# Optimization experiments

Measured on AMD Instinct MI355X. Metric: run time of the kernel, lower is better.

The kernel has to match this reference:

```python
import jax, jax.numpy as jnp
import numpy as np

N_NODES = 100000
N_EDGES = 1600000
IN_DIM = 64
HEADS = [4, 4]
DIMS = [16, 16]


def gat_layer(x, src, dst, W, al, ar, b, n_nodes):
    """DGL-style GATConv: x [N,F] -> [N,H,D]."""
    H, D = al.shape
    z = (x @ W).reshape(-1, H, D)                      # [N,H,D]
    el = jnp.sum(z * al, axis=-1)                      # [N,H]
    er = jnp.sum(z * ar, axis=-1)                      # [N,H]
    e = jax.nn.leaky_relu(el[src] + er[dst], 0.2)      # [E,H] edge scores
    # numerically-stable edge softmax over incoming edges of each dst node
    m = jax.ops.segment_max(e, dst, num_segments=n_nodes)
    m = jnp.where(jnp.isfinite(m), m, 0.0)
    ex = jnp.exp(e - jax.lax.stop_gradient(m)[dst])    # [E,H]
    denom = jax.ops.segment_sum(ex, dst, num_segments=n_nodes)
    alpha = ex / jnp.maximum(denom[dst], 1e-9)         # [E,H]
    # scatter-aggregate messages alpha * z[src]
    out = jax.ops.segment_sum(alpha[:, :, None] * z[src], dst, num_segments=n_nodes)
    return out + b.reshape(H, D)


def setup_inputs() -> dict:
    key = jax.random.key(0)
    ks = jax.random.split(key, 16)
    feat = jax.random.normal(ks[0], (N_NODES, IN_DIM), dtype=jnp.float32)
    src = jax.random.randint(ks[1], (N_EDGES,), 0, N_NODES, dtype=jnp.int32)
    dst = jax.random.randint(ks[2], (N_EDGES,), 0, N_NODES, dtype=jnp.int32)
    def lin(k, fi, fo):
        return jax.random.normal(k, (fi, fo), dtype=jnp.float32) * (1.0 / np.sqrt(fi))
    H0, D0 = HEADS[0], DIMS[0]
    H1, D1 = HEADS[1], DIMS[1]
    inp = {
        "feat": feat, "src": src, "dst": dst,
        "W0": lin(ks[3], IN_DIM, H0 * D0),
        "al0": jax.random.normal(ks[4], (H0, D0), jnp.float32) * 0.1,
        "ar0": jax.random.normal(ks[5], (H0, D0), jnp.float32) * 0.1,
        "b0": jnp.zeros((H0 * D0,), jnp.float32),
        "W1": lin(ks[6], H0 * D0, H1 * D1),
        "al1": jax.random.normal(ks[7], (H1, D1), jnp.float32) * 0.1,
        "ar1": jax.random.normal(ks[8], (H1, D1), jnp.float32) * 0.1,
        "b1": jnp.zeros((H1 * D1,), jnp.float32),
        "Wo": lin(ks[9], H1 * D1, 1),
        "alo": jax.random.normal(ks[10], (1, 1), jnp.float32) * 0.1,
        "aro": jax.random.normal(ks[11], (1, 1), jnp.float32) * 0.1,
        "bo": jnp.zeros((1,), jnp.float32),
    }
    return inp


def reference(feat, src, dst, W0, al0, ar0, b0, W1, al1, ar1, b1, Wo, alo, aro, bo):
    n = feat.shape[0]
    h = gat_layer(feat, src, dst, W0, al0, ar0, b0, n)       # [N,H0,D0]
    h = jax.nn.relu(h).reshape(n, -1)                         # head concat
    h = gat_layer(h, src, dst, W1, al1, ar1, b1, n)           # [N,H1,D1]
    h = jax.nn.relu(h).reshape(n, -1)
    out = gat_layer(h, src, dst, Wo, alo, aro, bo, n)         # [N,1,1]
    return jnp.squeeze(out, axis=1)                           # [N,1]
```

## Files before the change

### kernel.cpp

```cpp
#include <hip/hip_runtime.h>
#include <hip/hip_fp16.h>
#include <math.h>

#define NN 100000
#define NE 1600000
#define NBUK 391
#define CAP 4608
#define EPB 2048

__device__ __forceinline__ float leaky02(float v) {
    return v > 0.0f ? v : 0.2f * v;
}


__global__ __launch_bounds__(256) void k_bucket(
    const int* __restrict__ src, const int* __restrict__ dst,
    int* __restrict__ bucketCnt, int* __restrict__ gBuf)
{
    __shared__ int stg[EPB];
    __shared__ int tgt[EPB];
    __shared__ int lcnt[NBUK];
    __shared__ int lexc[NBUK];
    __shared__ int lgb[NBUK];
    __shared__ int totalLocal;
    const int t = threadIdx.x;
    const int e0 = blockIdx.x * EPB;

    for (int i = t; i < NBUK; i += 256) lcnt[i] = 0;
    __syncthreads();

    int bk[8], pk[8];
    #pragma unroll
    for (int j = 0; j < 8; ++j) {
        const int e = e0 + j * 256 + t;
        if (e < NE) {
            const int d = dst[e];
            bk[j] = d >> 8;
            pk[j] = (src[e] << 8) | (d & 255);
            atomicAdd(&lcnt[bk[j]], 1);
        } else bk[j] = -1;
    }
    __syncthreads();

    if (t < 64) {
        int carry = 0;
        for (int c = 0; c < NBUK; c += 64) {
            const int idx = c + t;
            int v = (idx < NBUK) ? lcnt[idx] : 0;
            int inc = v;
            #pragma unroll
            for (int off = 1; off < 64; off <<= 1) {
                int u = __shfl_up(inc, off, 64);
                if (t >= off) inc += u;
            }
            if (idx < NBUK) lexc[idx] = carry + inc - v;
            carry += __shfl(inc, 63, 64);
        }
        if (t == 0) totalLocal = carry;
    }
    __syncthreads();

    for (int i = t; i < NBUK; i += 256) {
        const int c = lcnt[i];
        lgb[i] = c ? atomicAdd(&bucketCnt[i], c) : 0;
        lcnt[i] = 0;
    }
    __syncthreads();

    #pragma unroll
    for (int j = 0; j < 8; ++j) {
        if (bk[j] >= 0) {
            const int r = atomicAdd(&lcnt[bk[j]], 1);
            const int p = lexc[bk[j]] + r;
            stg[p] = pk[j];
            int slot = lgb[bk[j]] + r;
            if (slot >= CAP) slot = CAP - 1;
            tgt[p] = bk[j] * CAP + slot;
        }
    }
    __syncthreads();

    const int tot = totalLocal;
    for (int i = t; i < tot; i += 256)
        gBuf[tgt[i]] = stg[i];
}

__global__ __launch_bounds__(256) void k_csr_local(
    const int* __restrict__ bucketCnt, const int* __restrict__ gBuf,
    int* __restrict__ row_ptr, int* __restrict__ ssrc)
{
    __shared__ int stg2[CAP];
    __shared__ int stg3[CAP];
    __shared__ int c2[256];
    __shared__ int sc[256];
    __shared__ int red[256];
    const int t = threadIdx.x;
    const int k = blockIdx.x;
    const int cnt = min(bucketCnt[k], CAP);

    int part = 0;
    for (int j = t; j < k; j += 256) part += bucketCnt[j];
    red[t] = part;
    __syncthreads();
    for (int s2 = 128; s2; s2 >>= 1) {
        if (t < s2) red[t] += red[t + s2];
        __syncthreads();
    }
    const int gb = red[0];

    c2[t] = 0;
    __syncthreads();
    for (int i = t; i < cnt; i += 256) {
        const int pk = gBuf[k * CAP + i];
        stg2[i] = pk;
        atomicAdd(&c2[pk & 255], 1);
    }
    __syncthreads();
    if (t < 64) {
        int carry = 0;
        for (int c = 0; c < 256; c += 64) {
            int v = c2[c + t];
            int inc = v;
            #pragma unroll
            for (int off = 1; off < 64; off <<= 1) {
                int u = __shfl_up(inc, off, 64);
                if (t >= off) inc += u;
            }
            sc[c + t] = carry + inc - v;
            carry += __shfl(inc, 63, 64);
        }
    }
    __syncthreads();
    const int node = (k << 8) + t;
    if (node < NN) row_ptr[node] = gb + sc[t];
    if (k == NBUK - 1 && t == 0) row_ptr[NN] = NE;
    c2[t] = 0;
    __syncthreads();
    for (int i = t; i < cnt; i += 256) {
        const int pk = stg2[i];
        const int dl = pk & 255;
        const int r = atomicAdd(&c2[dl], 1);
        stg3[sc[dl] + r] = pk >> 8;
    }
    __syncthreads();
    for (int i = t; i < cnt; i += 256)
        ssrc[gb + i] = stg3[i];
}


__global__ __launch_bounds__(256) void k_node_prep(
    const float* __restrict__ xin, const float* __restrict__ W,
    const float* __restrict__ al, const float* __restrict__ ar,
    __half* __restrict__ z, float* __restrict__ el, float* __restrict__ er)
{
    const int t = threadIdx.x;
    const int lane = t & 63;
    const int wvU = __builtin_amdgcn_readfirstlane(t >> 6);
    const int nodeBase = blockIdx.x * 64 + wvU * 16;

    float wc[64];
    #pragma unroll
    for (int k = 0; k < 64; ++k) wc[k] = W[k * 64 + lane];
    const float a_l = al[lane], a_r = ar[lane];

    #pragma unroll 1
    for (int i = 0; i < 16; i += 2) {
        const int nA = nodeBase + i;
        if (nA >= NN) break;
        const int nB = nA + 1;
        const bool hasB = (nB < NN);
        const float4* __restrict__ xA4 = (const float4*)(xin + (size_t)nA * 64);
        const float4* __restrict__ xB4 = (const float4*)(xin + (size_t)(hasB ? nB : nA) * 64);

        float accA = 0.f, accB = 0.f;
        #pragma unroll
        for (int k4 = 0; k4 < 16; ++k4) {
            const float4 a4 = xA4[k4];
            const float4 b4 = xB4[k4];
            const float w0 = wc[k4 * 4 + 0], w1 = wc[k4 * 4 + 1];
            const float w2 = wc[k4 * 4 + 2], w3 = wc[k4 * 4 + 3];
            accA += a4.x * w0 + a4.y * w1 + a4.z * w2 + a4.w * w3;
            accB += b4.x * w0 + b4.y * w1 + b4.z * w2 + b4.w * w3;
        }

        {
            z[(size_t)nA * 64 + lane] = __float2half(accA);
            float pl = accA * a_l, pr = accA * a_r;
            #pragma unroll
            for (int off = 8; off > 0; off >>= 1) {
                pl += __shfl_xor(pl, off, 16);
                pr += __shfl_xor(pr, off, 16);
            }
            if ((lane & 15) == 0) {
                const int h = lane >> 4;
                el[nA * 4 + h] = pl;
                er[nA * 4 + h] = pr;
            }
        }
        if (hasB) {
            z[(size_t)nB * 64 + lane] = __float2half(accB);
            float pl = accB * a_l, pr = accB * a_r;
            #pragma unroll
            for (int off = 8; off > 0; off >>= 1) {
                pl += __shfl_xor(pl, off, 16);
                pr += __shfl_xor(pr, off, 16);
            }
            if ((lane & 15) == 0) {
                const int h = lane >> 4;
                el[nB * 4 + h] = pl;
                er[nB * 4 + h] = pr;
            }
        }
    }
}

__global__ __launch_bounds__(256) void k_csr_agg(
    const int* __restrict__ row_ptr, const int* __restrict__ ssrc,
    const float* __restrict__ el, const float* __restrict__ er,
    const __half* __restrict__ z, const float* __restrict__ b,
    float* __restrict__ xout,
    const float* __restrict__ Wo,
    float* __restrict__ zo)
{
    const int t = threadIdx.x;
    const int wv = t >> 6, l = t & 63;
    const int sg = l >> 4, sl = l & 15;
    const int hh = sl >> 2;
    const int n = blockIdx.x * 4 + wv;
    const int beg = row_ptr[n], end = row_ptr[n + 1];
    const float er_hh = er[n * 4 + hh];

    float4 acc = {0.f, 0.f, 0.f, 0.f};
    float den = 0.f;
    int i = beg + sg;
    for (; i + 4 < end; i += 8) {
        const int s0 = ssrc[i], s1 = ssrc[i + 4];
        const float x0 = __expf(leaky02(el[s0 * 4 + hh] + er_hh));
        const float x1 = __expf(leaky02(el[s1 * 4 + hh] + er_hh));
        const uint2 r0 = *(const uint2*)(z + (size_t)s0 * 64 + sl * 4);
        const uint2 r1 = *(const uint2*)(z + (size_t)s1 * 64 + sl * 4);
        den += x0 + x1;
        const float2 p0 = __half22float2(*(const __half2*)&r0.x);
        const float2 q0 = __half22float2(*(const __half2*)&r0.y);
        const float2 p1 = __half22float2(*(const __half2*)&r1.x);
        const float2 q1 = __half22float2(*(const __half2*)&r1.y);
        acc.x += x0 * p0.x + x1 * p1.x;
        acc.y += x0 * p0.y + x1 * p1.y;
        acc.z += x0 * q0.x + x1 * q1.x;
        acc.w += x0 * q0.y + x1 * q1.y;
    }
    if (i < end) {
        const int s0 = ssrc[i];
        const float x0 = __expf(leaky02(el[s0 * 4 + hh] + er_hh));
        const uint2 r0 = *(const uint2*)(z + (size_t)s0 * 64 + sl * 4);
        den += x0;
        const float2 p0 = __half22float2(*(const __half2*)&r0.x);
        const float2 q0 = __half22float2(*(const __half2*)&r0.y);
        acc.x += x0 * p0.x; acc.y += x0 * p0.y;
        acc.z += x0 * q0.x; acc.w += x0 * q0.y;
    }

    #pragma unroll
    for (int off = 16; off < 64; off <<= 1) {
        acc.x += __shfl_xor(acc.x, off, 64);
        acc.y += __shfl_xor(acc.y, off, 64);
        acc.z += __shfl_xor(acc.z, off, 64);
        acc.w += __shfl_xor(acc.w, off, 64);
        den   += __shfl_xor(den,   off, 64);
    }
    const float dinv = 1.0f / fmaxf(den, 1e-9f);

    const float4 b4 = *(const float4*)(b + sl * 4);
    float4 v;
    v.x = fmaxf(acc.x * dinv + b4.x, 0.f);
    v.y = fmaxf(acc.y * dinv + b4.y, 0.f);
    v.z = fmaxf(acc.z * dinv + b4.z, 0.f);
    v.w = fmaxf(acc.w * dinv + b4.w, 0.f);

    if (xout) {
        if (l < 16) *(float4*)(xout + (size_t)n * 64 + sl * 4) = v;
    } else {
        const float4 w4 = *(const float4*)(Wo + sl * 4);
        float p = v.x * w4.x + v.y * w4.y + v.z * w4.z + v.w * w4.w;
        #pragma unroll
        for (int off = 1; off < 16; off <<= 1) p += __shfl_xor(p, off, 64);
        if (l == 0) zo[n] = p;
    }
}


__global__ __launch_bounds__(256) void k_csr_agg_o(
    const int* __restrict__ row_ptr, const int* __restrict__ ssrc,
    const float* __restrict__ zo, const float* __restrict__ alo,
    const float* __restrict__ aro, const float* __restrict__ bo,
    float* __restrict__ out)
{
    const int t = threadIdx.x, l = t & 15;
    const int n = blockIdx.x * 16 + (t >> 4);
    const float a = alo[0];
    const float zr = aro[0] * zo[n];
    const int beg = row_ptr[n], end = row_ptr[n + 1];

    float den = 0.f, accv = 0.f;
    for (int i = beg + l; i < end; i += 16) {
        const float zs = zo[ssrc[i]];
        const float ex = __expf(leaky02(a * zs + zr));
        den += ex; accv += ex * zs;
    }
    #pragma unroll
    for (int off = 8; off; off >>= 1) {
        den  += __shfl_xor(den, off, 16);
        accv += __shfl_xor(accv, off, 16);
    }
    if (l == 0) out[n] = accv / fmaxf(den, 1e-9f) + bo[0];
}


extern "C" void kernel_launch(void* const* d_in, const int* in_sizes, int n_in,
                              void* d_out, int out_size, void* d_ws, size_t ws_size,
                              hipStream_t stream) {
    const float* feat = (const float*)d_in[0];
    const int*   src  = (const int*)d_in[1];
    const int*   dst  = (const int*)d_in[2];
    const float* W0   = (const float*)d_in[3];
    const float* al0  = (const float*)d_in[4];
    const float* ar0  = (const float*)d_in[5];
    const float* b0   = (const float*)d_in[6];
    const float* W1   = (const float*)d_in[7];
    const float* al1  = (const float*)d_in[8];
    const float* ar1  = (const float*)d_in[9];
    const float* b1   = (const float*)d_in[10];
    const float* Wo   = (const float*)d_in[11];
    const float* alo  = (const float*)d_in[12];
    const float* aro  = (const float*)d_in[13];
    const float* bo   = (const float*)d_in[14];
    float* out = (float*)d_out;

    int* bucketCnt  = (int*)d_ws;
    int* row_ptr    = bucketCnt + NBUK;
    int* gBuf       = row_ptr + (NN + 2);
    int* ssrc       = gBuf + (size_t)NBUK * CAP;
    __half* z  = (__half*)(ssrc + NE);
    float* xA  = (float*)(z + (size_t)NN * 64);
    float* el  = xA + (size_t)NN * 64;
    float* er  = el + (size_t)NN * 4;
    float* zo  = er + (size_t)NN * 4;

    const int gBkt  = (NE + EPB - 1) / EPB;
    const int gPrep = (NN + 63) / 64;
    const int gN16  = NN / 16;
    const int gAgg  = NN / 4;

    hipMemsetAsync(bucketCnt, 0, NBUK * sizeof(int), stream);
    k_bucket   <<<gBkt, 256, 0, stream>>>(src, dst, bucketCnt, gBuf);
    k_csr_local<<<NBUK, 256, 0, stream>>>(bucketCnt, gBuf, row_ptr, ssrc);

    k_node_prep<<<gPrep, 256, 0, stream>>>(feat, W0, al0, ar0, z, el, er);
    k_csr_agg  <<<gAgg, 256, 0, stream>>>(row_ptr, ssrc, el, er, z, b0,
                                          xA, nullptr, nullptr);

    k_node_prep<<<gPrep, 256, 0, stream>>>(xA, W1, al1, ar1, z, el, er);
    k_csr_agg  <<<gAgg, 256, 0, stream>>>(row_ptr, ssrc, el, er, z, b1,
                                          nullptr, Wo, zo);

    k_csr_agg_o<<<gN16, 256, 0, stream>>>(row_ptr, ssrc, zo, alo, aro, bo, out);
}
```

Baseline: 280.5 us.

## Fuse layer-1 aggregation with layer-2 projection and deepen gather unrolling

The layer-1 aggregation kernel now applies the layer-2 linear projection and attention dot products in registers. This removes the fp32 intermediate write and the second node_prep launch, with the z, el and er buffers double-buffered between layers. The gather loop is unrolled to four edges per lane-group to expose more memory-level parallelism, and each wave now processes four nodes in sequence. The bucketing kernel handles 4096 edges per block. The fused kernel holds 64 weight registers per lane, which may lower occupancy.

```diff
diff --git a/kernel.cpp b/kernel.cpp
--- a/kernel.cpp
+++ b/kernel.cpp
@@ -6,7 +6,7 @@
 #define NE 1600000
 #define NBUK 391
 #define CAP 4608
-#define EPB 2048
+#define EPB 4096
 
 __device__ __forceinline__ float leaky02(float v) {
     return v > 0.0f ? v : 0.2f * v;
@@ -29,9 +29,9 @@
     for (int i = t; i < NBUK; i += 256) lcnt[i] = 0;
     __syncthreads();
 
-    int bk[8], pk[8];
-    #pragma unroll
-    for (int j = 0; j < 8; ++j) {
+    int bk[16], pk[16];
+    #pragma unroll
+    for (int j = 0; j < 16; ++j) {
         const int e = e0 + j * 256 + t;
         if (e < NE) {
             const int d = dst[e];
@@ -68,7 +68,7 @@
     __syncthreads();
 
     #pragma unroll
-    for (int j = 0; j < 8; ++j) {
+    for (int j = 0; j < 16; ++j) {
         if (bk[j] >= 0) {
             const int r = atomicAdd(&lcnt[bk[j]], 1);
             const int p = lexc[bk[j]] + r;
@@ -214,52 +214,46 @@
     }
 }
 
-__global__ __launch_bounds__(256) void k_csr_agg(
-    const int* __restrict__ row_ptr, const int* __restrict__ ssrc,
-    const float* __restrict__ el, const float* __restrict__ er,
-    const __half* __restrict__ z, const float* __restrict__ b,
-    float* __restrict__ xout,
-    const float* __restrict__ Wo,
-    float* __restrict__ zo)
-{
-    const int t = threadIdx.x;
-    const int wv = t >> 6, l = t & 63;
-    const int sg = l >> 4, sl = l & 15;
-    const int hh = sl >> 2;
-    const int n = blockIdx.x * 4 + wv;
-    const int beg = row_ptr[n], end = row_ptr[n + 1];
-    const float er_hh = er[n * 4 + hh];
-
-    float4 acc = {0.f, 0.f, 0.f, 0.f};
-    float den = 0.f;
+__device__ __forceinline__ void agg_gather(
+    const int beg, const int end, const int sg, const int sl, const int hh,
+    const float er_hh, const int* __restrict__ ssrc,
+    const float* __restrict__ el, const __half* __restrict__ z,
+    float4& acc, float& den)
+{
+    acc = make_float4(0.f, 0.f, 0.f, 0.f);
+    den = 0.f;
     int i = beg + sg;
-    for (; i + 4 < end; i += 8) {
+    for (; i + 12 < end; i += 16) {
         const int s0 = ssrc[i], s1 = ssrc[i + 4];
+        const int s2 = ssrc[i + 8], s3 = ssrc[i + 12];
         const float x0 = __expf(leaky02(el[s0 * 4 + hh] + er_hh));
         const float x1 = __expf(leaky02(el[s1 * 4 + hh] + er_hh));
+        const float x2 = __expf(leaky02(el[s2 * 4 + hh] + er_hh));
+        const float x3 = __expf(leaky02(el[s3 * 4 + hh] + er_hh));
         const uint2 r0 = *(const uint2*)(z + (size_t)s0 * 64 + sl * 4);
         const uint2 r1 = *(const uint2*)(z + (size_t)s1 * 64 + sl * 4);
-        den += x0 + x1;
-        const float2 p0 = __half22float2(*(const __half2*)&r0.x);
-        const float2 q0 = __half22float2(*(const __half2*)&r0.y);
-        const float2 p1 = __half22float2(*(const __half2*)&r1.x);
-        const float2 q1 = __half22float2(*(const __half2*)&r1.y);
-        acc.x += x0 * p0.x + x1 * p1.x;
-        acc.y += x0 * p0.y + x1 * p1.y;
-        acc.z += x0 * q0.x + x1 * q1.x;
-        acc.w += x0 * q0.y + x1 * q1.y;
-    }
-    if (i < end) {
+        const uint2 r2 = *(const uint2*)(z + (size_t)s2 * 64 + sl * 4);
+        const uint2 r3 = *(const uint2*)(z + (size_t)s3 * 64 + sl * 4);
+        den += (x0 + x1) + (x2 + x3);
+        float2 p;
+        p = __half22float2(*(const __half2*)&r0.x); acc.x += x0 * p.x; acc.y += x0 * p.y;
+        p = __half22float2(*(const __half2*)&r0.y); acc.z += x0 * p.x; acc.w += x0 * p.y;
+        p = __half22float2(*(const __half2*)&r1.x); acc.x += x1 * p.x; acc.y += x1 * p.y;
+        p = __half22float2(*(const __half2*)&r1.y); acc.z += x1 * p.x; acc.w += x1 * p.y;
+        p = __half22float2(*(const __half2*)&r2.x); acc.x += x2 * p.x; acc.y += x2 * p.y;
+        p = __half22float2(*(const __half2*)&r2.y); acc.z += x2 * p.x; acc.w += x2 * p.y;
+        p = __half22float2(*(const __half2*)&r3.x); acc.x += x3 * p.x; acc.y += x3 * p.y;
+        p = __half22float2(*(const __half2*)&r3.y); acc.z += x3 * p.x; acc.w += x3 * p.y;
+    }
+    for (; i < end; i += 4) {
         const int s0 = ssrc[i];
         const float x0 = __expf(leaky02(el[s0 * 4 + hh] + er_hh));
         const uint2 r0 = *(const uint2*)(z + (size_t)s0 * 64 + sl * 4);
         den += x0;
-        const float2 p0 = __half22float2(*(const __half2*)&r0.x);
-        const float2 q0 = __half22float2(*(const __half2*)&r0.y);
-        acc.x += x0 * p0.x; acc.y += x0 * p0.y;
-        acc.z += x0 * q0.x; acc.w += x0 * q0.y;
-    }
-
+        float2 p;
+        p = __half22float2(*(const __half2*)&r0.x); acc.x += x0 * p.x; acc.y += x0 * p.y;
+        p = __half22float2(*(const __half2*)&r0.y); acc.z += x0 * p.x; acc.w += x0 * p.y;
+    }
     #pragma unroll
     for (int off = 16; off < 64; off <<= 1) {
         acc.x += __shfl_xor(acc.x, off, 64);
@@ -268,19 +262,89 @@
         acc.w += __shfl_xor(acc.w, off, 64);
         den   += __shfl_xor(den,   off, 64);
     }
-    const float dinv = 1.0f / fmaxf(den, 1e-9f);
-
+}
+
+__global__ __launch_bounds__(256) void k_csr_agg_fuse(
+    const int* __restrict__ row_ptr, const int* __restrict__ ssrc,
+    const float* __restrict__ el, const float* __restrict__ er,
+    const __half* __restrict__ z, const float* __restrict__ b,
+    const float* __restrict__ Wn, const float* __restrict__ aln,
+    const float* __restrict__ arn,
+    __half* __restrict__ zn, float* __restrict__ eln, float* __restrict__ ern)
+{
+    const int t = threadIdx.x;
+    const int wv = t >> 6, l = t & 63;
+    const int sg = l >> 4, sl = l & 15, hh = sl >> 2;
+
+    float wcol[64];
+    #pragma unroll
+    for (int k = 0; k < 64; ++k) wcol[k] = Wn[k * 64 + l];
+    const float a_l = aln[l], a_r = arn[l];
     const float4 b4 = *(const float4*)(b + sl * 4);
-    float4 v;
-    v.x = fmaxf(acc.x * dinv + b4.x, 0.f);
-    v.y = fmaxf(acc.y * dinv + b4.y, 0.f);
-    v.z = fmaxf(acc.z * dinv + b4.z, 0.f);
-    v.w = fmaxf(acc.w * dinv + b4.w, 0.f);
-
-    if (xout) {
-        if (l < 16) *(float4*)(xout + (size_t)n * 64 + sl * 4) = v;
-    } else {
-        const float4 w4 = *(const float4*)(Wo + sl * 4);
+
+    #pragma unroll 1
+    for (int it = 0; it < 4; ++it) {
+        const int n = blockIdx.x * 16 + wv * 4 + it;
+        const int beg = row_ptr[n], end = row_ptr[n + 1];
+        const float er_hh = er[n * 4 + hh];
+        float4 acc; float den;
+        agg_gather(beg, end, sg, sl, hh, er_hh, ssrc, el, z, acc, den);
+        const float dinv = 1.0f / fmaxf(den, 1e-9f);
+        float4 v;
+        v.x = fmaxf(acc.x * dinv + b4.x, 0.f);
+        v.y = fmaxf(acc.y * dinv + b4.y, 0.f);
+        v.z = fmaxf(acc.z * dinv + b4.z, 0.f);
+        v.w = fmaxf(acc.w * dinv + b4.w, 0.f);
+
+        float zacc = 0.f;
+        #pragma unroll
+        for (int q = 0; q < 16; ++q) {
+            const float vx = __shfl(v.x, q, 64);
+            const float vy = __shfl(v.y, q, 64);
+            const float vz = __shfl(v.z, q, 64);
+            const float vw = __shfl(v.w, q, 64);
+            zacc += vx * wcol[4 * q + 0] + vy * wcol[4 * q + 1]
+                  + vz * wcol[4 * q + 2] + vw * wcol[4 * q + 3];
+        }
+        zn[(size_t)n * 64 + l] = __float2half(zacc);
+        float pl = zacc * a_l, pr = zacc * a_r;
+        #pragma unroll
+        for (int off = 8; off > 0; off >>= 1) {
+            pl += __shfl_xor(pl, off, 16);
+            pr += __shfl_xor(pr, off, 16);
+        }
+        if (sl == 0) {
+            eln[n * 4 + (l >> 4)] = pl;
+            ern[n * 4 + (l >> 4)] = pr;
+        }
+    }
+}
+
+__global__ __launch_bounds__(256) void k_csr_agg_out(
+    const int* __restrict__ row_ptr, const int* __restrict__ ssrc,
+    const float* __restrict__ el, const float* __restrict__ er,
+    const __half* __restrict__ z, const float* __restrict__ b,
+    const float* __restrict__ Wo, float* __restrict__ zo)
+{
+    const int t = threadIdx.x;
+    const int wv = t >> 6, l = t & 63;
+    const int sg = l >> 4, sl = l & 15, hh = sl >> 2;
+    const float4 b4 = *(const float4*)(b + sl * 4);
+    const float4 w4 = *(const float4*)(Wo + sl * 4);
+
+    #pragma unroll 1
+    for (int it = 0; it < 4; ++it) {
+        const int n = blockIdx.x * 16 + wv * 4 + it;
+        const int beg = row_ptr[n], end = row_ptr[n + 1];
+        const float er_hh = er[n * 4 + hh];
+        float4 acc; float den;
+        agg_gather(beg, end, sg, sl, hh, er_hh, ssrc, el, z, acc, den);
+        const float dinv = 1.0f / fmaxf(den, 1e-9f);
+        float4 v;
+        v.x = fmaxf(acc.x * dinv + b4.x, 0.f);
+        v.y = fmaxf(acc.y * dinv + b4.y, 0.f);
+        v.z = fmaxf(acc.z * dinv + b4.z, 0.f);
+        v.w = fmaxf(acc.w * dinv + b4.w, 0.f);
         float p = v.x * w4.x + v.y * w4.y + v.z * w4.z + v.w * w4.w;
         #pragma unroll
         for (int off = 1; off < 16; off <<= 1) p += __shfl_xor(p, off, 64);
@@ -340,28 +404,31 @@
     int* row_ptr    = bucketCnt + NBUK;
     int* gBuf       = row_ptr + (NN + 2);
     int* ssrc       = gBuf + (size_t)NBUK * CAP;
-    __half* z  = (__half*)(ssrc + NE);
-    float* xA  = (float*)(z + (size_t)NN * 64);
-    float* el  = xA + (size_t)NN * 64;
-    float* er  = el + (size_t)NN * 4;
-    float* zo  = er + (size_t)NN * 4;
+    uintptr_t pa = ((uintptr_t)(ssrc + NE) + 15) & ~(uintptr_t)15;
+    __half* zA = (__half*)pa;
+    __half* zB = zA + (size_t)NN * 64;
+    float* el0 = (float*)(zB + (size_t)NN * 64);
+    float* er0 = el0 + (size_t)NN * 4;
+    float* el1 = er0 + (size_t)NN * 4;
+    float* er1 = el1 + (size_t)NN * 4;
+    float* zo  = er1 + (size_t)NN * 4;
 
     const int gBkt  = (NE + EPB - 1) / EPB;
     const int gPrep = (NN + 63) / 64;
     const int gN16  = NN / 16;
-    const int gAgg  = NN / 4;
+    const int gAgg  = NN / 16;
 
     hipMemsetAsync(bucketCnt, 0, NBUK * sizeof(int), stream);
     k_bucket   <<<gBkt, 256, 0, stream>>>(src, dst, bucketCnt, gBuf);
     k_csr_local<<<NBUK, 256, 0, stream>>>(bucketCnt, gBuf, row_ptr, ssrc);
 
-    k_node_prep<<<gPrep, 256, 0, stream>>>(feat, W0, al0, ar0, z, el, er);
-    k_csr_agg  <<<gAgg, 256, 0, stream>>>(row_ptr, ssrc, el, er, z, b0,
-                                          xA, nullptr, nullptr);
-
-    k_node_prep<<<gPrep, 256, 0, stream>>>(xA, W1, al1, ar1, z, el, er);
-    k_csr_agg  <<<gAgg, 256, 0, stream>>>(row_ptr, ssrc, el, er, z, b1,
-                                          nullptr, Wo, zo);
+    k_node_prep<<<gPrep, 256, 0, stream>>>(feat, W0, al0, ar0, zA, el0, er0);
+
+    k_csr_agg_fuse<<<gAgg, 256, 0, stream>>>(row_ptr, ssrc, el0, er0, zA, b0,
+                                             W1, al1, ar1, zB, el1, er1);
+
+    k_csr_agg_out<<<gAgg, 256, 0, stream>>>(row_ptr, ssrc, el1, er1, zB, b1,
+                                            Wo, zo);
 
     k_csr_agg_o<<<gN16, 256, 0, stream>>>(row_ptr, ssrc, zo, alo, aro, bo, out);
 }
```

Measured after the change: 299.7 us. 6.8% more time.
